# Kernel optimization log

Measured on AMD Instinct MI355X. Metric: run time of the kernel, lower is better.

## Reference

```python
import jax, jax.numpy as jnp
import numpy as np

N = 1024
H = 4096
W = 4096
K_COUNTS = 10
IOU_T = 0.5
NEG = -1e30  # -inf stand-in for unrecorded groups


def _box_iou(b):
    # b: [N,4] xyxy pixel coords -> [N,N] IoU (torchvision.ops.box_iou)
    area = (b[:, 2] - b[:, 0]) * (b[:, 3] - b[:, 1])
    ix1 = jnp.maximum(b[:, None, 0], b[None, :, 0])
    iy1 = jnp.maximum(b[:, None, 1], b[None, :, 1])
    ix2 = jnp.minimum(b[:, None, 2], b[None, :, 2])
    iy2 = jnp.minimum(b[:, None, 3], b[None, :, 3])
    inter = jnp.clip(ix2 - ix1, 0.0) * jnp.clip(iy2 - iy1, 0.0)
    return inter / (area[:, None] + area[None, :] - inter)


def _c_wsl(iou_gt, scores, counts):
    # Faithful vectorized c_wsl_fast: for every start box i, greedily sweep
    # j = i+1..N-1 adding boxes compatible (IoU <= T) with all current members;
    # when a group hits `counts` at the TOP of a j-iteration it is recorded
    # (check-before-add semantics, so a group completed at j = N-1 is never
    # recorded, matching the original break-based control flow). The final
    # answer is the LAST start achieving the max recorded score (>= update).
    n = scores.shape[0]
    starts = jnp.arange(n)
    carry0 = (
        jnp.eye(n, dtype=bool),            # sel[i, k]: box k in group of start i
        jnp.ones(n, jnp.int32),            # group sizes
        scores,                            # group scores
        jnp.zeros(n, bool),                # recorded flag (== break)
        jnp.full(n, NEG, scores.dtype),    # recorded score
        jnp.zeros((n, n), bool),           # recorded membership
    )

    def step(c, xs):
        j, sj, iou_j = xs  # iou_j = iou_gt[j] (> T bool row; matrix symmetric)
        sel, size, score, rec, rec_score, rec_sel = c
        active = (j > starts) & (~rec)
        do_rec = active & (size == counts)
        rec_sel = jnp.where(do_rec[:, None], sel, rec_sel)
        rec_score = jnp.where(do_rec, score, rec_score)
        rec = rec | do_rec
        compat = ~jnp.any(sel & iou_j[None, :], axis=1)
        add = active & (~do_rec) & (size < counts) & compat
        sel = sel.at[:, j].set(sel[:, j] | add)
        size = size + add.astype(size.dtype)
        score = score + jnp.where(add, sj, jnp.zeros((), score.dtype))
        return (sel, size, score, rec, rec_score, rec_sel), None

    (_, _, _, rec, rec_score, rec_sel), _ = jax.lax.scan(
        step, carry0, (starts, scores, iou_gt))
    masked = jnp.where(rec, rec_score, NEG)
    best = (n - 1) - jnp.argmax(masked[::-1])  # last argmax == '>=' update rule
    return jnp.where(jnp.any(rec), rec_sel[best], jnp.zeros(n, bool))


def reference(bbox, obj_scores, probs, counts):
    Hh, Ww = probs.shape
    # score_bbox_heatmap(reduction='mean'): mean of probs[y1:y2, x1:x2] per box,
    # computed exactly for all boxes with a zero-padded summed-area table.
    sat = jnp.pad(jnp.cumsum(jnp.cumsum(probs, axis=0), axis=1), ((1, 0), (1, 0)))
    x1 = jnp.clip(jnp.floor(bbox[:, 0]).astype(jnp.int32), 0, Ww)
    y1 = jnp.clip(jnp.floor(bbox[:, 1]).astype(jnp.int32), 0, Hh)
    x2 = jnp.clip(jnp.floor(bbox[:, 2]).astype(jnp.int32), 0, Ww)
    y2 = jnp.clip(jnp.floor(bbox[:, 3]).astype(jnp.int32), 0, Hh)
    sums = sat[y2, x2] - sat[y1, x2] - sat[y2, x1] + sat[y1, x1]
    cnt = jnp.maximum((y2 - y1) * (x2 - x1), 1).astype(probs.dtype)
    box_scores = sums / cnt
    # agg_score_method == 'mean'
    scores = 0.5 * (obj_scores + box_scores)
    # sort descending, then greedy IoU grouping on sorted boxes
    order = jnp.argsort(-scores)
    bbox_s = bbox[order]
    scores_s = scores[order]
    iou_gt = _box_iou(bbox_s) > IOU_T
    sel = _c_wsl(iou_gt, scores_s, counts)
    return scores_s * sel.astype(scores_s.dtype)


def setup_inputs() -> dict:
    key = jax.random.key(0)
    k1, k2, k3, k4, k5, k6 = jax.random.split(key, 6)
    cx = jax.random.uniform(k1, (N,), minval=0.15, maxval=0.85) * W
    cy = jax.random.uniform(k2, (N,), minval=0.15, maxval=0.85) * H
    bw = jnp.maximum(jax.random.uniform(k3, (N,), minval=0.02, maxval=0.25) * W, 8.0)
    bh = jnp.maximum(jax.random.uniform(k4, (N,), minval=0.02, maxval=0.25) * H, 8.0)
    bbox = jnp.stack([cx - bw / 2, cy - bh / 2, cx + bw / 2, cy + bh / 2], axis=1)
    obj_scores = jax.random.uniform(k5, (N,))
    probs = jax.random.uniform(k6, (H, W))
    return {"bbox": bbox, "obj_scores": obj_scores, "probs": probs, "counts": K_COUNTS}
```

## Files before the change

kernel.cpp:

```cpp
#include <hip/hip_runtime.h>

#define HH 4096
#define WW 4096
#define NB 1024
#define NCHUNK 256
#define CROWS 16
#define IOU_T 0.5f
#define NBLK_STAGE 1024
#define NBLK_TAIL 256

typedef unsigned long long u64;

constexpr size_t OFF_PART   = 0;
constexpr size_t OFF_SC64   = OFF_PART   + (size_t)NCHUNK * WW * 8;
constexpr size_t OFF_ORDER  = OFF_SC64   + (size_t)NB * 8;
constexpr size_t OFF_CTR    = OFF_ORDER  + (size_t)NB * 4;
constexpr size_t OFF_IOU    = OFF_CTR    + 4096;
constexpr size_t OFF_RECSC  = OFF_IOU    + (size_t)NB * 16 * 8;
constexpr size_t OFF_RECSEL = OFF_RECSC  + (size_t)NB * 8;
constexpr size_t OFF_CC     = OFF_RECSEL + (size_t)NB * 16 * 8;
constexpr size_t OFF_PART2  = OFF_CC     + (size_t)HH * WW * 4;

template <typename T>
__device__ __forceinline__ void st_c(T* p, T v) {
    __hip_atomic_store(p, v, __ATOMIC_RELAXED, __HIP_MEMORY_SCOPE_AGENT);
}

__device__ __forceinline__ void gbar(int* bctr, int round) {
    asm volatile("s_waitcnt vmcnt(0)" ::: "memory");
    __syncthreads();
    if (threadIdx.x == 0) {
        __hip_atomic_fetch_add(bctr, 1, __ATOMIC_RELAXED, __HIP_MEMORY_SCOPE_AGENT);
        while (__hip_atomic_load(bctr, __ATOMIC_RELAXED, __HIP_MEMORY_SCOPE_AGENT)
               < NBLK_TAIL * round)
            __builtin_amdgcn_s_sleep(2);
    }
    __syncthreads();
}


__global__ void __launch_bounds__(256) k_stage(const float* __restrict__ probs,
        const float* __restrict__ bbox,
        double* __restrict__ part, double* __restrict__ part2,
        float* __restrict__ Cc, int* __restrict__ ctrs) {
    __shared__ int xlo_s[CROWS], xhi_s[CROWS];
    __shared__ int2 rng_s[CROWS];
    __shared__ int sIdx;
    int tid = blockIdx.x * 256 + threadIdx.x;
    int c  = tid >> 10;
    int xq = tid & 1023;
    int t  = threadIdx.x;
    if (t < CROWS) { xlo_s[t] = WW + 1; xhi_s[t] = -1; }
    __syncthreads();
    int r0 = c * CROWS;
    for (int i = t; i < NB; i += 256) {
        float4 bb = ((const float4*)bbox)[i];
        int x1 = min(max((int)floorf(bb.x), 0), WW);
        int y1 = min(max((int)floorf(bb.y), 0), HH);
        int x2 = min(max((int)floorf(bb.z), 0), WW);
        int y2 = min(max((int)floorf(bb.w), 0), HH);
        int ra = y1 - 1 - r0, rb = y2 - 1 - r0;
        if (ra >= 0 && ra < CROWS) { atomicMin(&xlo_s[ra], x1); atomicMax(&xhi_s[ra], x2); }
        if (rb >= 0 && rb < CROWS) { atomicMin(&xlo_s[rb], x1); atomicMax(&xhi_s[rb], x2); }
    }
    __syncthreads();
    if (t < CROWS) {
        int lo = xlo_s[t], hi = xhi_s[t];
        rng_s[t] = (hi >= 0) ? make_int2(lo >> 2, (hi + 3) >> 2) : make_int2(1, 0);
    }
    __syncthreads();
    const float4* p = (const float4*)probs + (size_t)r0 * (WW / 4) + xq;
    float4* Cc4 = (float4*)Cc;
    double a0 = 0.0, a1 = 0.0, a2 = 0.0, a3 = 0.0;
    for (int r = 0; r < CROWS; r += 8) {
        float4 q[8];
        #pragma unroll
        for (int k = 0; k < 8; k++) q[k] = p[(size_t)(r + k) * (WW / 4)];
        #pragma unroll
        for (int k = 0; k < 8; k++) {
            a0 += (double)q[k].x; a1 += (double)q[k].y;
            a2 += (double)q[k].z; a3 += (double)q[k].w;
            int2 d = rng_s[r + k];
            if (xq >= d.x && xq < d.y)
                Cc4[(size_t)(r0 + r + k) * (WW / 4) + xq] =
                    make_float4((float)a0, (float)a1, (float)a2, (float)a3);
        }
    }
    size_t pbase = (size_t)c * WW + 4 * (size_t)xq;
    st_c(&part[pbase + 0], a0);
    st_c(&part[pbase + 1], a1);
    st_c(&part[pbase + 2], a2);
    st_c(&part[pbase + 3], a3);

    asm volatile("s_waitcnt vmcnt(0)" ::: "memory");
    __syncthreads();
    if (t == 0)
        sIdx = __hip_atomic_fetch_add(&ctrs[16 * ((blockIdx.x & 15) + 1)], 1,
                                      __ATOMIC_RELAXED, __HIP_MEMORY_SCOPE_AGENT);
    __syncthreads();
    if (sIdx != 63) return;
    if (t == 0) {
        for (;;) {
            int s = 0;
            for (int i2 = 0; i2 < 16; i2++)
                s += __hip_atomic_load(&ctrs[16 * (i2 + 1)], __ATOMIC_RELAXED,
                                       __HIP_MEMORY_SCOPE_AGENT);
            if (s == NBLK_STAGE) break;
            __builtin_amdgcn_s_sleep(2);
        }
    }
    __syncthreads();
    {
        int x = (blockIdx.x & 15) * 256 + t;
        double carry = 0.0;
        for (int g = 0; g < NCHUNK / 16; g++) {
            double v[16];
            #pragma unroll
            for (int k = 0; k < 16; k++) v[k] = part[(size_t)(g * 16 + k) * WW + x];
            #pragma unroll
            for (int k = 0; k < 16; k++) { double tv = v[k]; v[k] = carry; carry += tv; }
            #pragma unroll
            for (int k = 0; k < 16; k++) part2[(size_t)(g * 16 + k) * WW + x] = v[k];
        }
    }
}

__global__ void __launch_bounds__(1024) k_tail(const float* __restrict__ bbox,
        const float* __restrict__ obj,
        const float* __restrict__ Cc,
        const double* __restrict__ part2,
        const int* __restrict__ counts,
        double* __restrict__ sc64, int* __restrict__ order,
        u64* __restrict__ ioub, double* __restrict__ recsc,
        u64* __restrict__ recsel, int* __restrict__ ctrs,
        float* __restrict__ out) {
    __shared__ double s_sc[NB];
    __shared__ int    ord_s[NB];
    __shared__ alignas(16) u64 big[NB * 16];
    __shared__ double red[16];
    __shared__ int    redi[16];
    float4* sbb = (float4*)big;
    int b = blockIdx.x, t = threadIdx.x;
    int* bctr = &ctrs[0];

    {
        int bg = t >> 8;
        int tl = t & 255;
        int i = b * 4 + bg;
        float4 bb = ((const float4*)bbox)[i];
        int x1 = min(max((int)floorf(bb.x), 0), WW);
        int y1 = min(max((int)floorf(bb.y), 0), HH);
        int x2 = min(max((int)floorf(bb.z), 0), WW);
        int y2 = min(max((int)floorf(bb.w), 0), HH);
        bool h1 = (y1 >= 1), h2 = (y2 >= 1);
        const float*  r2 = Cc    + (size_t)(h2 ? (y2 - 1) : 0) * WW;
        const double* q2 = part2 + (size_t)(h2 ? ((y2 - 1) >> 4) : 0) * WW;
        const float*  r1 = Cc    + (size_t)(h1 ? (y1 - 1) : 0) * WW;
        const double* q1 = part2 + (size_t)(h1 ? ((y1 - 1) >> 4) : 0) * WW;
        double s = 0.0;
        for (int x = x1 + tl; x < x2; x += 256) {
            double v2 = h2 ? ((double)r2[x] + q2[x]) : 0.0;
            double v1 = h1 ? ((double)r1[x] + q1[x]) : 0.0;
            s += (v2 - v1);
        }
        #pragma unroll
        for (int off = 32; off > 0; off >>= 1) s += __shfl_down(s, off);
        if ((t & 63) == 0) red[t >> 6] = s;
        __syncthreads();
        if (tl == 0) {
            double tot = red[bg * 4] + red[bg * 4 + 1] + red[bg * 4 + 2] + red[bg * 4 + 3];
            long long cnt = (long long)(y2 - y1) * (long long)(x2 - x1);
            if (cnt < 1) cnt = 1;
            st_c(&sc64[i], 0.5 * ((double)obj[i] + tot / (double)cnt));
        }
    }
    gbar(bctr, 1);

    s_sc[t] = sc64[t];
    __syncthreads();
    {
        int bg = t >> 8;
        int tl = t & 255;
        int i = b * 4 + bg;
        double si = s_sc[i];
        int p = 0;
        #pragma unroll
        for (int it = 0; it < 4; it++) {
            int j = tl * 4 + it;
            double sj = s_sc[j];
            p += (sj > si) || (sj == si && j < i);
        }
        #pragma unroll
        for (int off = 32; off > 0; off >>= 1) p += __shfl_down(p, off);
        if ((t & 63) == 0) redi[t >> 6] = p;
        __syncthreads();
        if (t < 4) {
            int r = redi[t * 4] + redi[t * 4 + 1] + redi[t * 4 + 2] + redi[t * 4 + 3];
            st_c(&order[r], b * 4 + t);
        }
    }
    gbar(bctr, 2);

    {
        int o = order[t];
        ord_s[t] = o;
        sbb[t] = ((const float4*)bbox)[o];
    }
    __syncthreads();
    {
        int l = t & 63;
        for (int task = t >> 6; task < 64; task += 16) {
            int r = task >> 4, wd = task & 15;
            int i = b * 4 + r;
            float4 a = sbb[i];
            float ai = (a.z - a.x) * (a.w - a.y);
            float4 bb = sbb[(wd << 6) + l];
            float aj = (bb.z - bb.x) * (bb.w - bb.y);
            float ix1 = fmaxf(a.x, bb.x), iy1 = fmaxf(a.y, bb.y);
            float ix2 = fminf(a.z, bb.z), iy2 = fminf(a.w, bb.w);
            float iw = fmaxf(ix2 - ix1, 0.0f), ih = fmaxf(iy2 - iy1, 0.0f);
            float inter = iw * ih;
            float iou_v = inter / (ai + aj - inter);
            u64 m = __ballot(iou_v > IOU_T);
            if (l == 0) st_c(&ioub[(size_t)i * 16 + wd], m);
        }
    }
    gbar(bctr, 3);

    #pragma unroll
    for (int k = 0; k < 16; k++) big[t + k * 1024] = ioub[t + k * 1024];
    __syncthreads();
    {
        int K = counts[0];
        if (t < 4) {
            int i = b * 4 + t;
            u64 inc[16], sel[16];
            int wi = i >> 6, bi = i & 63;
            #pragma unroll
            for (int w = 0; w < 16; w++) {
                inc[w] = big[i * 16 + w];
                sel[w] = (w == wi) ? (1ULL << bi) : 0ULL;
            }
            int size = 1;
            double score = s_sc[ord_s[i]];
            int last = i;
            #pragma unroll
            for (int w = 0; w < 16; w++) {
                if (w < wi || size >= K) continue;
                u64 avail = ~inc[w];
                if (w == wi) avail &= (bi == 63) ? 0ULL : (~0ULL << (bi + 1));
                while (avail != 0ULL && size < K) {
                    int bj = __builtin_ctzll(avail);
                    int j = (w << 6) + bj;
                    sel[w] |= 1ULL << bj;
                    size++;
                    score += s_sc[ord_s[j]];
                    last = j;
                    const u64* rj = &big[j * 16];
                    #pragma unroll
                    for (int w2 = 0; w2 < 16; w2++) inc[w2] |= rj[w2];
                    avail &= ~inc[w];
                    avail &= ~(1ULL << bj);
                }
            }
            int rec = (size == K) && (last < NB - 1);
            st_c(&recsc[i], rec ? score : -1e300);
            #pragma unroll
            for (int w = 0; w < 16; w++) st_c(&recsel[(size_t)i * 16 + w], sel[w]);
        }
    }
    gbar(bctr, 4);
    if (b != 0) return;

    if (t < 64) {
        double bs = -1e301; int bidx = 0;
        for (int m = 0; m < 16; m++) {
            int k = t * 16 + m;
            double v = recsc[k];
            if (v >= bs) { bs = v; bidx = k; }
        }
        #pragma unroll
        for (int off = 32; off > 0; off >>= 1) {
            double ob = __shfl_down(bs, off);
            int oi = __shfl_down(bidx, off);
            if (ob > bs || (ob == bs && oi > bidx)) { bs = ob; bidx = oi; }
        }
        bs = __shfl(bs, 0);
        bidx = __shfl(bidx, 0);
        int any = bs > -1e299;
        for (int k = t; k < NB; k += 64) {
            float v = 0.0f;
            if (any && ((recsel[(size_t)bidx * 16 + (k >> 6)] >> (k & 63)) & 1ULL))
                v = (float)s_sc[ord_s[k]];
            out[k] = v;
        }
    }
}


extern "C" void kernel_launch(void* const* d_in, const int* in_sizes, int n_in,
                              void* d_out, int out_size, void* d_ws, size_t ws_size,
                              hipStream_t stream) {
    const float* bbox  = (const float*)d_in[0];
    const float* obj   = (const float*)d_in[1];
    const float* probs = (const float*)d_in[2];
    const int*   counts = (const int*)d_in[3];
    float* out = (float*)d_out;

    char* w = (char*)d_ws;
    double* part    = (double*)(w + OFF_PART);
    double* sc64    = (double*)(w + OFF_SC64);
    int*    order   = (int*)(w + OFF_ORDER);
    int*    ctrs    = (int*)(w + OFF_CTR);
    u64*    ioub    = (u64*)(w + OFF_IOU);
    double* recsc   = (double*)(w + OFF_RECSC);
    u64*    recsel  = (u64*)(w + OFF_RECSEL);
    float*  Cc      = (float*)(w + OFF_CC);
    double* part2   = (double*)(w + OFF_PART2);

    hipMemsetAsync(w + OFF_CTR, 0, 4096, stream);
    k_stage<<<NBLK_STAGE, 256, 0, stream>>>(probs, bbox, part, part2, Cc, ctrs);
    k_tail<<<NBLK_TAIL, 1024, 0, stream>>>(bbox, obj, Cc, part2, counts,
                                           sc64, order, ioub, recsc,
                                           recsel, ctrs, out);
}
```

Before: 166.5 us.

## Fuse stage and tail kernels into one persistent kernel with grid barriers

Merges the column-prefix stage kernel into the persistent tail kernel, so a single 256x1024 launch does the chunk sums, the cross-chunk scan and the grouping. The removed kernel boundary and launch gap are replaced by a new per-XCD hierarchical barrier that issues an L2 writeback (buffer_wbl2), followed by an extra grid barrier after the scan. The trade-offs: each block now streams 16 rows with 1024 threads instead of 1024 smaller blocks, the scan runs on only 16 blocks while the rest wait, and the kernel now relies on all 256 blocks being co-resident.

```diff
diff --git a/kernel.cpp b/kernel.cpp
--- a/kernel.cpp
+++ b/kernel.cpp
@@ -6,8 +6,8 @@
 #define NCHUNK 256
 #define CROWS 16
 #define IOU_T 0.5f
-#define NBLK_STAGE 1024
-#define NBLK_TAIL 256
+#define NBLK 256
+#define NTHR 1024
 
 typedef unsigned long long u64;
 
@@ -26,114 +26,53 @@
     __hip_atomic_store(p, v, __ATOMIC_RELAXED, __HIP_MEMORY_SCOPE_AGENT);
 }
 
-__device__ __forceinline__ void gbar(int* bctr, int round) {
+__device__ __forceinline__ void gbar(int* ctrs, int round) {
     asm volatile("s_waitcnt vmcnt(0)" ::: "memory");
     __syncthreads();
     if (threadIdx.x == 0) {
-        __hip_atomic_fetch_add(bctr, 1, __ATOMIC_RELAXED, __HIP_MEMORY_SCOPE_AGENT);
-        while (__hip_atomic_load(bctr, __ATOMIC_RELAXED, __HIP_MEMORY_SCOPE_AGENT)
-               < NBLK_TAIL * round)
+        __hip_atomic_fetch_add(&ctrs[0], 1, __ATOMIC_RELAXED, __HIP_MEMORY_SCOPE_AGENT);
+        while (__hip_atomic_load(&ctrs[0], __ATOMIC_RELAXED, __HIP_MEMORY_SCOPE_AGENT)
+               < NBLK * round)
             __builtin_amdgcn_s_sleep(2);
     }
     __syncthreads();
 }
 
-
-__global__ void __launch_bounds__(256) k_stage(const float* __restrict__ probs,
+__device__ __forceinline__ void fbar(int* ctrs, int round) {
+    asm volatile("s_waitcnt vmcnt(0)" ::: "memory");
+    __syncthreads();
+    if (threadIdx.x == 0) {
+        unsigned xcc;
+        asm volatile("s_getreg_b32 %0, hwreg(HW_REG_XCC_ID)" : "=s"(xcc));
+        int first = __hip_atomic_fetch_add(&ctrs[32 + (xcc & 7)], 1,
+                                           __ATOMIC_RELAXED, __HIP_MEMORY_SCOPE_AGENT);
+        __hip_atomic_fetch_add(&ctrs[0], 1, __ATOMIC_RELAXED, __HIP_MEMORY_SCOPE_AGENT);
+        if (first == 0) {
+            while (__hip_atomic_load(&ctrs[0], __ATOMIC_RELAXED, __HIP_MEMORY_SCOPE_AGENT)
+                   < NBLK * round)
+                __builtin_amdgcn_s_sleep(2);
+            asm volatile("buffer_wbl2" ::: "memory");
+            asm volatile("s_waitcnt vmcnt(0)" ::: "memory");
+            __hip_atomic_fetch_add(&ctrs[16], 1, __ATOMIC_RELAXED, __HIP_MEMORY_SCOPE_AGENT);
+        }
+        while (__hip_atomic_load(&ctrs[16], __ATOMIC_RELAXED, __HIP_MEMORY_SCOPE_AGENT) < 8)
+            __builtin_amdgcn_s_sleep(2);
+    }
+    __syncthreads();
+}
+
+__global__ void __launch_bounds__(1024) k_all(const float* __restrict__ probs,
         const float* __restrict__ bbox,
+        const float* __restrict__ obj,
+        const int* __restrict__ counts,
         double* __restrict__ part, double* __restrict__ part2,
-        float* __restrict__ Cc, int* __restrict__ ctrs) {
-    __shared__ int xlo_s[CROWS], xhi_s[CROWS];
-    __shared__ int2 rng_s[CROWS];
-    __shared__ int sIdx;
-    int tid = blockIdx.x * 256 + threadIdx.x;
-    int c  = tid >> 10;
-    int xq = tid & 1023;
-    int t  = threadIdx.x;
-    if (t < CROWS) { xlo_s[t] = WW + 1; xhi_s[t] = -1; }
-    __syncthreads();
-    int r0 = c * CROWS;
-    for (int i = t; i < NB; i += 256) {
-        float4 bb = ((const float4*)bbox)[i];
-        int x1 = min(max((int)floorf(bb.x), 0), WW);
-        int y1 = min(max((int)floorf(bb.y), 0), HH);
-        int x2 = min(max((int)floorf(bb.z), 0), WW);
-        int y2 = min(max((int)floorf(bb.w), 0), HH);
-        int ra = y1 - 1 - r0, rb = y2 - 1 - r0;
-        if (ra >= 0 && ra < CROWS) { atomicMin(&xlo_s[ra], x1); atomicMax(&xhi_s[ra], x2); }
-        if (rb >= 0 && rb < CROWS) { atomicMin(&xlo_s[rb], x1); atomicMax(&xhi_s[rb], x2); }
-    }
-    __syncthreads();
-    if (t < CROWS) {
-        int lo = xlo_s[t], hi = xhi_s[t];
-        rng_s[t] = (hi >= 0) ? make_int2(lo >> 2, (hi + 3) >> 2) : make_int2(1, 0);
-    }
-    __syncthreads();
-    const float4* p = (const float4*)probs + (size_t)r0 * (WW / 4) + xq;
-    float4* Cc4 = (float4*)Cc;
-    double a0 = 0.0, a1 = 0.0, a2 = 0.0, a3 = 0.0;
-    for (int r = 0; r < CROWS; r += 8) {
-        float4 q[8];
-        #pragma unroll
-        for (int k = 0; k < 8; k++) q[k] = p[(size_t)(r + k) * (WW / 4)];
-        #pragma unroll
-        for (int k = 0; k < 8; k++) {
-            a0 += (double)q[k].x; a1 += (double)q[k].y;
-            a2 += (double)q[k].z; a3 += (double)q[k].w;
-            int2 d = rng_s[r + k];
-            if (xq >= d.x && xq < d.y)
-                Cc4[(size_t)(r0 + r + k) * (WW / 4) + xq] =
-                    make_float4((float)a0, (float)a1, (float)a2, (float)a3);
-        }
-    }
-    size_t pbase = (size_t)c * WW + 4 * (size_t)xq;
-    st_c(&part[pbase + 0], a0);
-    st_c(&part[pbase + 1], a1);
-    st_c(&part[pbase + 2], a2);
-    st_c(&part[pbase + 3], a3);
-
-    asm volatile("s_waitcnt vmcnt(0)" ::: "memory");
-    __syncthreads();
-    if (t == 0)
-        sIdx = __hip_atomic_fetch_add(&ctrs[16 * ((blockIdx.x & 15) + 1)], 1,
-                                      __ATOMIC_RELAXED, __HIP_MEMORY_SCOPE_AGENT);
-    __syncthreads();
-    if (sIdx != 63) return;
-    if (t == 0) {
-        for (;;) {
-            int s = 0;
-            for (int i2 = 0; i2 < 16; i2++)
-                s += __hip_atomic_load(&ctrs[16 * (i2 + 1)], __ATOMIC_RELAXED,
-                                       __HIP_MEMORY_SCOPE_AGENT);
-            if (s == NBLK_STAGE) break;
-            __builtin_amdgcn_s_sleep(2);
-        }
-    }
-    __syncthreads();
-    {
-        int x = (blockIdx.x & 15) * 256 + t;
-        double carry = 0.0;
-        for (int g = 0; g < NCHUNK / 16; g++) {
-            double v[16];
-            #pragma unroll
-            for (int k = 0; k < 16; k++) v[k] = part[(size_t)(g * 16 + k) * WW + x];
-            #pragma unroll
-            for (int k = 0; k < 16; k++) { double tv = v[k]; v[k] = carry; carry += tv; }
-            #pragma unroll
-            for (int k = 0; k < 16; k++) part2[(size_t)(g * 16 + k) * WW + x] = v[k];
-        }
-    }
-}
-
-__global__ void __launch_bounds__(1024) k_tail(const float* __restrict__ bbox,
-        const float* __restrict__ obj,
-        const float* __restrict__ Cc,
-        const double* __restrict__ part2,
-        const int* __restrict__ counts,
+        float* __restrict__ Cc,
         double* __restrict__ sc64, int* __restrict__ order,
         u64* __restrict__ ioub, double* __restrict__ recsc,
         u64* __restrict__ recsel, int* __restrict__ ctrs,
         float* __restrict__ out) {
+    __shared__ int xlo_s[CROWS], xhi_s[CROWS];
+    __shared__ int2 rng_s[CROWS];
     __shared__ double s_sc[NB];
     __shared__ int    ord_s[NB];
     __shared__ alignas(16) u64 big[NB * 16];
@@ -141,7 +80,65 @@
     __shared__ int    redi[16];
     float4* sbb = (float4*)big;
     int b = blockIdx.x, t = threadIdx.x;
-    int* bctr = &ctrs[0];
+
+    {
+        if (t < CROWS) { xlo_s[t] = WW + 1; xhi_s[t] = -1; }
+        __syncthreads();
+        int r0 = b * CROWS;
+        {
+            float4 bb = ((const float4*)bbox)[t];
+            int x1 = min(max((int)floorf(bb.x), 0), WW);
+            int y1 = min(max((int)floorf(bb.y), 0), HH);
+            int x2 = min(max((int)floorf(bb.z), 0), WW);
+            int y2 = min(max((int)floorf(bb.w), 0), HH);
+            int ra = y1 - 1 - r0, rb = y2 - 1 - r0;
+            if (ra >= 0 && ra < CROWS) { atomicMin(&xlo_s[ra], x1); atomicMax(&xhi_s[ra], x2); }
+            if (rb >= 0 && rb < CROWS) { atomicMin(&xlo_s[rb], x1); atomicMax(&xhi_s[rb], x2); }
+        }
+        __syncthreads();
+        if (t < CROWS) {
+            int lo = xlo_s[t], hi = xhi_s[t];
+            rng_s[t] = (hi >= 0) ? make_int2(lo >> 2, (hi + 3) >> 2) : make_int2(1, 0);
+        }
+        __syncthreads();
+        const float4* p = (const float4*)probs + (size_t)r0 * (WW / 4) + t;
+        float4* Cc4 = (float4*)Cc;
+        double a0 = 0.0, a1 = 0.0, a2 = 0.0, a3 = 0.0;
+        for (int r = 0; r < CROWS; r += 8) {
+            float4 q[8];
+            #pragma unroll
+            for (int k = 0; k < 8; k++) q[k] = p[(size_t)(r + k) * (WW / 4)];
+            #pragma unroll
+            for (int k = 0; k < 8; k++) {
+                a0 += (double)q[k].x; a1 += (double)q[k].y;
+                a2 += (double)q[k].z; a3 += (double)q[k].w;
+                int2 d = rng_s[r + k];
+                if (t >= d.x && t < d.y)
+                    Cc4[(size_t)(r0 + r + k) * (WW / 4) + t] =
+                        make_float4((float)a0, (float)a1, (float)a2, (float)a3);
+            }
+        }
+        double2* pp = (double2*)(part + (size_t)b * WW) + t * 2;
+        pp[0] = make_double2(a0, a1);
+        pp[1] = make_double2(a2, a3);
+    }
+    fbar(ctrs, 1);
+
+    if (b < 16 && t < 256) {
+        int x = b * 256 + t;
+        double carry = 0.0;
+        for (int g = 0; g < NCHUNK / 16; g++) {
+            double v[16];
+            #pragma unroll
+            for (int k = 0; k < 16; k++) v[k] = part[(size_t)(g * 16 + k) * WW + x];
+            #pragma unroll
+            for (int k = 0; k < 16; k++) { double tv = v[k]; v[k] = carry; carry += tv; }
+            #pragma unroll
+            for (int k = 0; k < 16; k++)
+                st_c(&part2[(size_t)(g * 16 + k) * WW + x], v[k]);
+        }
+    }
+    gbar(ctrs, 2);
 
     {
         int bg = t >> 8;
@@ -174,7 +171,7 @@
             st_c(&sc64[i], 0.5 * ((double)obj[i] + tot / (double)cnt));
         }
     }
-    gbar(bctr, 1);
+    gbar(ctrs, 3);
 
     s_sc[t] = sc64[t];
     __syncthreads();
@@ -199,7 +196,7 @@
             st_c(&order[r], b * 4 + t);
         }
     }
-    gbar(bctr, 2);
+    gbar(ctrs, 4);
 
     {
         int o = order[t];
@@ -225,7 +222,7 @@
             if (l == 0) st_c(&ioub[(size_t)i * 16 + wd], m);
         }
     }
-    gbar(bctr, 3);
+    gbar(ctrs, 5);
 
     #pragma unroll
     for (int k = 0; k < 16; k++) big[t + k * 1024] = ioub[t + k * 1024];
@@ -269,7 +266,7 @@
             for (int w = 0; w < 16; w++) st_c(&recsel[(size_t)i * 16 + w], sel[w]);
         }
     }
-    gbar(bctr, 4);
+    gbar(ctrs, 6);
     if (b != 0) return;
 
     if (t < 64) {
@@ -319,8 +316,7 @@
     double* part2   = (double*)(w + OFF_PART2);
 
     hipMemsetAsync(w + OFF_CTR, 0, 4096, stream);
-    k_stage<<<NBLK_STAGE, 256, 0, stream>>>(probs, bbox, part, part2, Cc, ctrs);
-    k_tail<<<NBLK_TAIL, 1024, 0, stream>>>(bbox, obj, Cc, part2, counts,
-                                           sc64, order, ioub, recsc,
-                                           recsel, ctrs, out);
-}
+    k_all<<<NBLK, NTHR, 0, stream>>>(probs, bbox, obj, counts, part, part2,
+                                     Cc, sc64, order, ioub, recsc, recsel,
+                                     ctrs, out);
+}
```

Measured after the change: 174.5 us. +4.8%, slower.
